# Performance work log

Hardware: AMD Instinct MI355X
Metric: run time of the kernel (lower is better)

The kernel has to match this reference:

```python
import jax, jax.numpy as jnp
import numpy as np

B, S, D = 16, 2048, 128


def setup_inputs() -> dict:
    key = jax.random.key(0)
    kq, kk, kv = jax.random.split(key, 3)
    return {
        "queries": jax.random.normal(kq, (B, S, D), dtype=jnp.float32),
        "keys": jax.random.normal(kk, (B, S, D), dtype=jnp.float32),
        "values": jax.random.normal(kv, (B, S, D), dtype=jnp.float32),
        "mask": jnp.zeros((B, S, S), dtype=bool),  # True -> masked out
    }


def reference(queries, keys, values, mask):
    d_k = queries.shape[-1]
    scale = 1.0 / np.sqrt(d_k).astype(np.float32)
    # scores: [B, S, S]
    scores = jnp.einsum("bqd,bkd->bqk", queries, keys) * scale
    scores = jnp.where(mask, -jnp.inf, scores)
    attn_weights = jax.nn.softmax(scores, axis=-1)
    # dropout prob = 0.0 (eval), identity
    output = jnp.einsum("bqk,bkd->bqd", attn_weights, values)
    return output
```

## Files before the change

kernel.cpp:

```cpp
#include <hip/hip_runtime.h>
#include <hip/hip_bf16.h>

#define SEQ    2048
#define DIM    128
#define NBATCH 16
#define KVB    64
#define HALFS  (SEQ / 2)
#define NTILE  (HALFS / KVB)
#define QW     32
#define NWAVE  4
#define QB     (QW * NWAVE)
#define NROW   (NBATCH * SEQ)
#define TELEM  (KVB * DIM)

typedef __bf16 bf16x8 __attribute__((ext_vector_type(8)));
typedef float  f32x4  __attribute__((ext_vector_type(4)));
typedef unsigned int uint;

#define LOG2E  1.44269504088896340736f
#define NEGINF (-__builtin_inff())

#define CVT_PK(d, lo, hi) asm("v_cvt_pk_bf16_f32 %0, %1, %2" : "=v"(d) : "v"(lo), "v"(hi))
#define SWAP32(x, y) asm("v_permlane32_swap_b32 %0, %1" : "+v"(x), "+v"(y))
#define SWAP16(x, y) asm("v_permlane16_swap_b32 %0, %1" : "+v"(x), "+v"(y))

typedef const __attribute__((address_space(1))) uint* gup;
typedef       __attribute__((address_space(3))) uint* lup;
#define GLDS16(g, l) __builtin_amdgcn_global_load_lds((gup)(g), (lup)(l), 16, 0, 0)

#define APPLY_MASK(mw, s)                          \
    if (mw) {                                      \
        if (mw & 0x000000ffu) s[0] = NEGINF;       \
        if (mw & 0x0000ff00u) s[1] = NEGINF;       \
        if (mw & 0x00ff0000u) s[2] = NEGINF;       \
        if (mw & 0xff000000u) s[3] = NEGINF;       \
    }

__global__ __launch_bounds__(512)
void sdpa_prep(const float* __restrict__ Kg, const float* __restrict__ Vg,
               __bf16* __restrict__ Kb, __bf16* __restrict__ Vb)
{
    const int tile = (int)blockIdx.x;
    const int tid  = (int)threadIdx.x;
    const size_t row0 = (size_t)tile * KVB;

    {
        const int kr = tid >> 3;
        const int c2 = (tid & 7) * 2;
        const int kx = kr & 7;
        const float* src = Kg + (row0 + kr) * DIM;
        __bf16* dst = Kb + ((size_t)tile * KVB + kr) * DIM;
        #pragma unroll
        for (int c = 0; c < 2; ++c) {
            const int ci = c2 + c;
            const int sc = ci ^ kx;
            const float4 a = *(const float4*)(src + sc * 8);
            const float4 b = *(const float4*)(src + sc * 8 + 4);
            bf16x8 h;
            h[0]=(__bf16)a.x; h[1]=(__bf16)a.y; h[2]=(__bf16)a.z; h[3]=(__bf16)a.w;
            h[4]=(__bf16)b.x; h[5]=(__bf16)b.y; h[6]=(__bf16)b.z; h[7]=(__bf16)b.w;
            *(bf16x8*)(dst + ci * 8) = h;
        }
    }
    {
        const int vd  = tid & 127;
        const int vks = tid >> 7;
        const int vx  = vd & 7;
        const float* src = Vg + row0 * DIM + vd;
        __bf16* dst = Vb + (size_t)tile * TELEM + (size_t)vd * KVB;
        #pragma unroll
        for (int c = 0; c < 2; ++c) {
            const int ck = vks * 2 + c;
            const int ci = ck ^ vx;
            bf16x8 h;
            #pragma unroll
            for (int j = 0; j < 8; ++j) h[j] = (__bf16)src[(size_t)(ck * 8 + j) * DIM];
            *(bf16x8*)(dst + ci * 8) = h;
        }
    }
}

__global__ __launch_bounds__(256, 2)
void sdpa_main(const float* __restrict__ Qg, const __bf16* __restrict__ Kbf,
               const __bf16* __restrict__ Vbf, const unsigned char* __restrict__ Mg,
               float* __restrict__ Uw, float* __restrict__ Lw)
{
    __shared__ __bf16 Ksh[2][TELEM];
    __shared__ __bf16 Vsh[2][TELEM];

    const int tid  = (int)threadIdx.x;
    const int wid  = tid >> 6;
    const int lane = tid & 63;
    const int lg   = lane >> 4;
    const int lr   = lane & 15;

    const int bid  = (int)blockIdx.x;
    const int nbid = (bid & 7) * 64 + (bid >> 3);
    const int half = nbid & 1;
    const int qt   = nbid >> 1;
    const int bb   = qt >> 4;
    const int q0w  = (qt & 15) * QB + wid * QW;

    const float qscale = 0.08838834764831845f * LOG2E;

    bf16x8 aqA[4], aqB[4];
    #pragma unroll
    for (int g = 0; g < 2; ++g) {
        const float* qrow = Qg + ((size_t)(bb * SEQ + q0w + g * 16 + lr)) * DIM;
        #pragma unroll
        for (int kb = 0; kb < 4; ++kb) {
            const float4 f0 = *(const float4*)(qrow + kb * 32 + lg * 8);
            const float4 f1 = *(const float4*)(qrow + kb * 32 + lg * 8 + 4);
            bf16x8 h;
            h[0] = (__bf16)(f0.x * qscale); h[1] = (__bf16)(f0.y * qscale);
            h[2] = (__bf16)(f0.z * qscale); h[3] = (__bf16)(f0.w * qscale);
            h[4] = (__bf16)(f1.x * qscale); h[5] = (__bf16)(f1.y * qscale);
            h[6] = (__bf16)(f1.z * qscale); h[7] = (__bf16)(f1.w * qscale);
            if (g == 0) aqA[kb] = h; else aqB[kb] = h;
        }
    }

    const __bf16* Kt0 = Kbf + (size_t)(bb * 32 + half * 16) * TELEM;
    const __bf16* Vt0 = Vbf + (size_t)(bb * 32 + half * 16) * TELEM;
    const unsigned char* MrowA = Mg + (size_t)bb * SEQ * SEQ
                               + (size_t)(q0w + lr) * SEQ + half * HALFS;
    const unsigned char* MrowB = MrowA + (size_t)16 * SEQ;

    uint mA0, mA1, mA2, mA3, mB0, mB1, mB2, mB3;
    const int loff = lane * 16;

    auto issue = [&](int t, int b) {
        const char* Ks = (const char*)(Kt0 + (size_t)t * TELEM);
        const char* Vs = (const char*)(Vt0 + (size_t)t * TELEM);
        char* Kd = (char*)Ksh[b];
        char* Vd = (char*)Vsh[b];
        #pragma unroll
        for (int j = 0; j < 4; ++j) {
            const int o = wid * 1024 + j * 4096;
            GLDS16(Ks + o + loff, Kd + o);
            GLDS16(Vs + o + loff, Vd + o);
        }
        const unsigned char* msA = MrowA + t * KVB + lg * 4;
        mA0 = *(const uint*)(msA);
        mA1 = *(const uint*)(msA + 16);
        mA2 = *(const uint*)(msA + 32);
        mA3 = *(const uint*)(msA + 48);
        const unsigned char* msB = MrowB + t * KVB + lg * 4;
        mB0 = *(const uint*)(msB);
        mB1 = *(const uint*)(msB + 16);
        mB2 = *(const uint*)(msB + 32);
        mB3 = *(const uint*)(msB + 48);
    };

    issue(0, 0);

    f32x4 accA[8], accB[8];
    #pragma unroll
    for (int i = 0; i < 8; ++i) { accA[i] = (f32x4)(0.0f); accB[i] = (f32x4)(0.0f); }
    float lA = 0.0f, lB = 0.0f;

    const int kxr = lr & 7;

    for (int t = 0; t < NTILE; ++t) {
        asm volatile("s_waitcnt vmcnt(0)" ::: "memory");
        __syncthreads();
        const uint wA0 = mA0, wA1 = mA1, wA2 = mA2, wA3 = mA3;
        const uint wB0 = mB0, wB1 = mB1, wB2 = mB2, wB3 = mB3;
        if (t + 1 < NTILE) issue(t + 1, (t + 1) & 1);

        const bf16x8* const Kc = (const bf16x8*)Ksh[t & 1];
        const bf16x8* const Vc = (const bf16x8*)Vsh[t & 1];

        f32x4 sA0 = (f32x4)(0.0f), sA1 = (f32x4)(0.0f);
        f32x4 sA2 = (f32x4)(0.0f), sA3 = (f32x4)(0.0f);
        f32x4 sB0 = (f32x4)(0.0f), sB1 = (f32x4)(0.0f);
        f32x4 sB2 = (f32x4)(0.0f), sB3 = (f32x4)(0.0f);
        __builtin_amdgcn_s_setprio(1);
        #pragma unroll
        for (int kb = 0; kb < 4; ++kb) {
            const int ch = (kb * 4 + lg) ^ kxr;
            const bf16x8 a0 = Kc[(lr)      * 16 + ch];
            const bf16x8 a1 = Kc[(16 + lr) * 16 + ch];
            const bf16x8 a2 = Kc[(32 + lr) * 16 + ch];
            const bf16x8 a3 = Kc[(48 + lr) * 16 + ch];
            sA0 = __builtin_amdgcn_mfma_f32_16x16x32_bf16(a0, aqA[kb], sA0, 0, 0, 0);
            sB0 = __builtin_amdgcn_mfma_f32_16x16x32_bf16(a0, aqB[kb], sB0, 0, 0, 0);
            sA1 = __builtin_amdgcn_mfma_f32_16x16x32_bf16(a1, aqA[kb], sA1, 0, 0, 0);
            sB1 = __builtin_amdgcn_mfma_f32_16x16x32_bf16(a1, aqB[kb], sB1, 0, 0, 0);
            sA2 = __builtin_amdgcn_mfma_f32_16x16x32_bf16(a2, aqA[kb], sA2, 0, 0, 0);
            sB2 = __builtin_amdgcn_mfma_f32_16x16x32_bf16(a2, aqB[kb], sB2, 0, 0, 0);
            sA3 = __builtin_amdgcn_mfma_f32_16x16x32_bf16(a3, aqA[kb], sA3, 0, 0, 0);
            sB3 = __builtin_amdgcn_mfma_f32_16x16x32_bf16(a3, aqB[kb], sB3, 0, 0, 0);
        }
        __builtin_amdgcn_s_setprio(0);

        APPLY_MASK(wA0, sA0) APPLY_MASK(wA1, sA1) APPLY_MASK(wA2, sA2) APPLY_MASK(wA3, sA3)
        APPLY_MASK(wB0, sB0) APPLY_MASK(wB1, sB1) APPLY_MASK(wB2, sB2) APPLY_MASK(wB3, sB3)

        float psA = 0.0f, psB = 0.0f;
        #pragma unroll
        for (int r = 0; r < 4; ++r) { sA0[r] = __builtin_amdgcn_exp2f(sA0[r]); psA += sA0[r]; }
        #pragma unroll
        for (int r = 0; r < 4; ++r) { sA1[r] = __builtin_amdgcn_exp2f(sA1[r]); psA += sA1[r]; }
        #pragma unroll
        for (int r = 0; r < 4; ++r) { sA2[r] = __builtin_amdgcn_exp2f(sA2[r]); psA += sA2[r]; }
        #pragma unroll
        for (int r = 0; r < 4; ++r) { sA3[r] = __builtin_amdgcn_exp2f(sA3[r]); psA += sA3[r]; }
        #pragma unroll
        for (int r = 0; r < 4; ++r) { sB0[r] = __builtin_amdgcn_exp2f(sB0[r]); psB += sB0[r]; }
        #pragma unroll
        for (int r = 0; r < 4; ++r) { sB1[r] = __builtin_amdgcn_exp2f(sB1[r]); psB += sB1[r]; }
        #pragma unroll
        for (int r = 0; r < 4; ++r) { sB2[r] = __builtin_amdgcn_exp2f(sB2[r]); psB += sB2[r]; }
        #pragma unroll
        for (int r = 0; r < 4; ++r) { sB3[r] = __builtin_amdgcn_exp2f(sB3[r]); psB += sB3[r]; }
        lA += psA;
        lB += psB;

        bf16x8 apA0, apA1, apB0, apB1;
        {
            uint a0w, a1w, b0w, b1w, c0w, c1w, d0w, d1w;
            CVT_PK(a0w, sA0[0], sA0[1]); CVT_PK(a1w, sA0[2], sA0[3]);
            CVT_PK(b0w, sA1[0], sA1[1]); CVT_PK(b1w, sA1[2], sA1[3]);
            CVT_PK(c0w, sA2[0], sA2[1]); CVT_PK(c1w, sA2[2], sA2[3]);
            CVT_PK(d0w, sA3[0], sA3[1]); CVT_PK(d1w, sA3[2], sA3[3]);
            SWAP32(a0w, b0w); SWAP16(a0w, b0w);
            SWAP32(a1w, b1w); SWAP16(a1w, b1w);
            SWAP32(c0w, d0w); SWAP16(c0w, d0w);
            SWAP32(c1w, d1w); SWAP16(c1w, d1w);
            union W { uint w[4]; bf16x8 v; };
            W u0, u1;
            u0.w[0] = a0w; u0.w[1] = a1w; u0.w[2] = b0w; u0.w[3] = b1w;
            u1.w[0] = c0w; u1.w[1] = c1w; u1.w[2] = d0w; u1.w[3] = d1w;
            apA0 = u0.v; apA1 = u1.v;
        }
        {
            uint a0w, a1w, b0w, b1w, c0w, c1w, d0w, d1w;
            CVT_PK(a0w, sB0[0], sB0[1]); CVT_PK(a1w, sB0[2], sB0[3]);
            CVT_PK(b0w, sB1[0], sB1[1]); CVT_PK(b1w, sB1[2], sB1[3]);
            CVT_PK(c0w, sB2[0], sB2[1]); CVT_PK(c1w, sB2[2], sB2[3]);
            CVT_PK(d0w, sB3[0], sB3[1]); CVT_PK(d1w, sB3[2], sB3[3]);
            SWAP32(a0w, b0w); SWAP16(a0w, b0w);
            SWAP32(a1w, b1w); SWAP16(a1w, b1w);
            SWAP32(c0w, d0w); SWAP16(c0w, d0w);
            SWAP32(c1w, d1w); SWAP16(c1w, d1w);
            union W { uint w[4]; bf16x8 v; };
            W u0, u1;
            u0.w[0] = a0w; u0.w[1] = a1w; u0.w[2] = b0w; u0.w[3] = b1w;
            u1.w[0] = c0w; u1.w[1] = c1w; u1.w[2] = d0w; u1.w[3] = d1w;
            apB0 = u0.v; apB1 = u1.v;
        }

        __builtin_amdgcn_s_setprio(1);
        #pragma unroll
        for (int nt = 0; nt < 8; ++nt) {
            const int rowb = (nt * 16 + lr) * 8;
            const bf16x8 bv0 = Vc[rowb + (lg ^ kxr)];
            const bf16x8 bv1 = Vc[rowb + ((4 + lg) ^ kxr)];
            accA[nt] = __builtin_amdgcn_mfma_f32_16x16x32_bf16(apA0, bv0, accA[nt], 0, 0, 0);
            accA[nt] = __builtin_amdgcn_mfma_f32_16x16x32_bf16(apA1, bv1, accA[nt], 0, 0, 0);
            accB[nt] = __builtin_amdgcn_mfma_f32_16x16x32_bf16(apB0, bv0, accB[nt], 0, 0, 0);
            accB[nt] = __builtin_amdgcn_mfma_f32_16x16x32_bf16(apB1, bv1, accB[nt], 0, 0, 0);
        }
        __builtin_amdgcn_s_setprio(0);
    }

    lA += __shfl_xor(lA, 16); lA += __shfl_xor(lA, 32);
    lB += __shfl_xor(lB, 16); lB += __shfl_xor(lB, 32);
    if (lg == 0) {
        Lw[(size_t)half * NROW + bb * SEQ + q0w + lr]      = lA;
        Lw[(size_t)half * NROW + bb * SEQ + q0w + 16 + lr] = lB;
    }

    float* ubA = Uw + ((size_t)half * NROW + bb * SEQ + q0w + lg * 4) * DIM + lr;
    float* ubB = ubA + (size_t)16 * DIM;
    #pragma unroll
    for (int r = 0; r < 4; ++r)
        #pragma unroll
        for (int nt = 0; nt < 8; ++nt) {
            ubA[(size_t)r * DIM + nt * 16] = accA[nt][r];
            ubB[(size_t)r * DIM + nt * 16] = accB[nt][r];
        }
}

__global__ __launch_bounds__(256)
void sdpa_combine(float* __restrict__ Og, const float* __restrict__ Uw,
                  const float* __restrict__ Lw)
{
    const int gid = (int)blockIdx.x * 256 + (int)threadIdx.x;
    const int row = gid >> 5;
    const float inv = 1.0f / (Lw[row] + Lw[NROW + row]);
    const float4* U0 = (const float4*)Uw;
    const float4* U1 = (const float4*)(Uw + (size_t)NROW * DIM);
    const float4 a = U0[gid];
    const float4 b = U1[gid];
    float4 o;
    o.x = (a.x + b.x) * inv; o.y = (a.y + b.y) * inv;
    o.z = (a.z + b.z) * inv; o.w = (a.w + b.w) * inv;
    ((float4*)Og)[gid] = o;
}

extern "C" void kernel_launch(void* const* d_in, const int* in_sizes, int n_in,
                              void* d_out, int out_size, void* d_ws, size_t ws_size,
                              hipStream_t stream) {
    const float* Q = (const float*)d_in[0];
    const float* K = (const float*)d_in[1];
    const float* V = (const float*)d_in[2];
    const unsigned char* M = (const unsigned char*)d_in[3];
    float* O  = (float*)d_out;
    float*  Uw  = (float*)d_ws;
    float*  Lw  = Uw + (size_t)2 * NROW * DIM;
    __bf16* Kbf = (__bf16*)(Lw + 2 * NROW);
    __bf16* Vbf = Kbf + (size_t)NROW * DIM;
    sdpa_prep<<<dim3(NROW / KVB), dim3(512), 0, stream>>>(K, V, Kbf, Vbf);
    sdpa_main<<<dim3(512), dim3(256), 0, stream>>>(Q, Kbf, Vbf, M, Uw, Lw);
    sdpa_combine<<<dim3(NROW * DIM / 4 / 256), dim3(256), 0, stream>>>(O, Uw, Lw);
}
```

Measured before the change: 76.44 us.

## Split KV sequence into four parts with 32-row tiles for more blocks

Splits the key/value range four ways instead of two, doubling the main-kernel grid to 1024 blocks, and shrinks KV tiles from 64 to 32 rows. This halves LDS use per block and raises the occupancy hint to 3 blocks per CU, aiming to fill the GPU better and hide latency. The cost is more partial-output traffic: four fp32 slabs are written and then read back in the combine kernel. Each tile also does less MFMA work per barrier, so per-tile sync overhead grows relative to compute. The V layout swizzle is changed to match the narrower tile.

After: 91.88 us. 20.2% more time.

```diff
diff --git a/kernel.cpp b/kernel.cpp
--- a/kernel.cpp
+++ b/kernel.cpp
@@ -4,9 +4,10 @@
 #define SEQ    2048
 #define DIM    128
 #define NBATCH 16
-#define KVB    64
-#define HALFS  (SEQ / 2)
-#define NTILE  (HALFS / KVB)
+#define KVB    32
+#define NSPLIT 4
+#define QUART  (SEQ / NSPLIT)
+#define NTILE  (QUART / KVB)
 #define QW     32
 #define NWAVE  4
 #define QB     (QW * NWAVE)
@@ -36,7 +37,7 @@
         if (mw & 0xff000000u) s[3] = NEGINF;       \
     }
 
-__global__ __launch_bounds__(512)
+__global__ __launch_bounds__(256)
 void sdpa_prep(const float* __restrict__ Kg, const float* __restrict__ Vg,
                __bf16* __restrict__ Kb, __bf16* __restrict__ Vb)
 {
@@ -49,7 +50,7 @@
         const int c2 = (tid & 7) * 2;
         const int kx = kr & 7;
         const float* src = Kg + (row0 + kr) * DIM;
-        __bf16* dst = Kb + ((size_t)tile * KVB + kr) * DIM;
+        __bf16* dst = Kb + (size_t)tile * TELEM + (size_t)kr * DIM;
         #pragma unroll
         for (int c = 0; c < 2; ++c) {
             const int ci = c2 + c;
@@ -63,14 +64,14 @@
         }
     }
     {
-        const int vd  = tid & 127;
-        const int vks = tid >> 7;
-        const int vx  = vd & 7;
+        const int vd = tid & 127;
+        const int cp = (tid >> 7) * 2;
+        const int vx = (vd >> 1) & 3;
         const float* src = Vg + row0 * DIM + vd;
         __bf16* dst = Vb + (size_t)tile * TELEM + (size_t)vd * KVB;
         #pragma unroll
         for (int c = 0; c < 2; ++c) {
-            const int ck = vks * 2 + c;
+            const int ck = cp + c;
             const int ci = ck ^ vx;
             bf16x8 h;
             #pragma unroll
@@ -80,7 +81,7 @@
     }
 }
 
-__global__ __launch_bounds__(256, 2)
+__global__ __launch_bounds__(256, 3)
 void sdpa_main(const float* __restrict__ Qg, const __bf16* __restrict__ Kbf,
                const __bf16* __restrict__ Vbf, const unsigned char* __restrict__ Mg,
                float* __restrict__ Uw, float* __restrict__ Lw)
@@ -95,18 +96,19 @@
     const int lr   = lane & 15;
 
     const int bid  = (int)blockIdx.x;
-    const int nbid = (bid & 7) * 64 + (bid >> 3);
-    const int half = nbid & 1;
-    const int qt   = nbid >> 1;
-    const int bb   = qt >> 4;
-    const int q0w  = (qt & 15) * QB + wid * QW;
+    const int nbid = (bid & 7) * 128 + (bid >> 3);
+    const int qtl  = nbid & 15;
+    const int g    = nbid >> 4;
+    const int quar = g & 3;
+    const int bb   = g >> 2;
+    const int q0w  = qtl * QB + wid * QW;
 
     const float qscale = 0.08838834764831845f * LOG2E;
 
     bf16x8 aqA[4], aqB[4];
     #pragma unroll
-    for (int g = 0; g < 2; ++g) {
-        const float* qrow = Qg + ((size_t)(bb * SEQ + q0w + g * 16 + lr)) * DIM;
+    for (int gq = 0; gq < 2; ++gq) {
+        const float* qrow = Qg + ((size_t)(bb * SEQ + q0w + gq * 16 + lr)) * DIM;
         #pragma unroll
         for (int kb = 0; kb < 4; ++kb) {
             const float4 f0 = *(const float4*)(qrow + kb * 32 + lg * 8);
@@ -116,17 +118,17 @@
             h[2] = (__bf16)(f0.z * qscale); h[3] = (__bf16)(f0.w * qscale);
             h[4] = (__bf16)(f1.x * qscale); h[5] = (__bf16)(f1.y * qscale);
             h[6] = (__bf16)(f1.z * qscale); h[7] = (__bf16)(f1.w * qscale);
-            if (g == 0) aqA[kb] = h; else aqB[kb] = h;
-        }
-    }
-
-    const __bf16* Kt0 = Kbf + (size_t)(bb * 32 + half * 16) * TELEM;
-    const __bf16* Vt0 = Vbf + (size_t)(bb * 32 + half * 16) * TELEM;
+            if (gq == 0) aqA[kb] = h; else aqB[kb] = h;
+        }
+    }
+
+    const __bf16* Kt0 = Kbf + (size_t)(bb * 64 + quar * 16) * TELEM;
+    const __bf16* Vt0 = Vbf + (size_t)(bb * 64 + quar * 16) * TELEM;
     const unsigned char* MrowA = Mg + (size_t)bb * SEQ * SEQ
-                               + (size_t)(q0w + lr) * SEQ + half * HALFS;
+                               + (size_t)(q0w + lr) * SEQ + quar * QUART;
     const unsigned char* MrowB = MrowA + (size_t)16 * SEQ;
 
-    uint mA0, mA1, mA2, mA3, mB0, mB1, mB2, mB3;
+    uint mA0, mA1, mB0, mB1;
     const int loff = lane * 16;
 
     auto issue = [&](int t, int b) {
@@ -135,7 +137,7 @@
         char* Kd = (char*)Ksh[b];
         char* Vd = (char*)Vsh[b];
         #pragma unroll
-        for (int j = 0; j < 4; ++j) {
+        for (int j = 0; j < 2; ++j) {
             const int o = wid * 1024 + j * 4096;
             GLDS16(Ks + o + loff, Kd + o);
             GLDS16(Vs + o + loff, Vd + o);
@@ -143,13 +145,9 @@
         const unsigned char* msA = MrowA + t * KVB + lg * 4;
         mA0 = *(const uint*)(msA);
         mA1 = *(const uint*)(msA + 16);
-        mA2 = *(const uint*)(msA + 32);
-        mA3 = *(const uint*)(msA + 48);
         const unsigned char* msB = MrowB + t * KVB + lg * 4;
         mB0 = *(const uint*)(msB);
         mB1 = *(const uint*)(msB + 16);
-        mB2 = *(const uint*)(msB + 32);
-        mB3 = *(const uint*)(msB + 48);
     };
 
     issue(0, 0);
@@ -160,42 +158,34 @@
     float lA = 0.0f, lB = 0.0f;
 
     const int kxr = lr & 7;
+    const int vxr = (lr >> 1) & 3;
 
     for (int t = 0; t < NTILE; ++t) {
         asm volatile("s_waitcnt vmcnt(0)" ::: "memory");
         __syncthreads();
-        const uint wA0 = mA0, wA1 = mA1, wA2 = mA2, wA3 = mA3;
-        const uint wB0 = mB0, wB1 = mB1, wB2 = mB2, wB3 = mB3;
+        const uint wA0 = mA0, wA1 = mA1, wB0 = mB0, wB1 = mB1;
         if (t + 1 < NTILE) issue(t + 1, (t + 1) & 1);
 
         const bf16x8* const Kc = (const bf16x8*)Ksh[t & 1];
         const bf16x8* const Vc = (const bf16x8*)Vsh[t & 1];
 
         f32x4 sA0 = (f32x4)(0.0f), sA1 = (f32x4)(0.0f);
-        f32x4 sA2 = (f32x4)(0.0f), sA3 = (f32x4)(0.0f);
         f32x4 sB0 = (f32x4)(0.0f), sB1 = (f32x4)(0.0f);
-        f32x4 sB2 = (f32x4)(0.0f), sB3 = (f32x4)(0.0f);
         __builtin_amdgcn_s_setprio(1);
         #pragma unroll
         for (int kb = 0; kb < 4; ++kb) {
             const int ch = (kb * 4 + lg) ^ kxr;
             const bf16x8 a0 = Kc[(lr)      * 16 + ch];
             const bf16x8 a1 = Kc[(16 + lr) * 16 + ch];
-            const bf16x8 a2 = Kc[(32 + lr) * 16 + ch];
-            const bf16x8 a3 = Kc[(48 + lr) * 16 + ch];
             sA0 = __builtin_amdgcn_mfma_f32_16x16x32_bf16(a0, aqA[kb], sA0, 0, 0, 0);
             sB0 = __builtin_amdgcn_mfma_f32_16x16x32_bf16(a0, aqB[kb], sB0, 0, 0, 0);
             sA1 = __builtin_amdgcn_mfma_f32_16x16x32_bf16(a1, aqA[kb], sA1, 0, 0, 0);
             sB1 = __builtin_amdgcn_mfma_f32_16x16x32_bf16(a1, aqB[kb], sB1, 0, 0, 0);
-            sA2 = __builtin_amdgcn_mfma_f32_16x16x32_bf16(a2, aqA[kb], sA2, 0, 0, 0);
-            sB2 = __builtin_amdgcn_mfma_f32_16x16x32_bf16(a2, aqB[kb], sB2, 0, 0, 0);
-            sA3 = __builtin_amdgcn_mfma_f32_16x16x32_bf16(a3, aqA[kb], sA3, 0, 0, 0);
-            sB3 = __builtin_amdgcn_mfma_f32_16x16x32_bf16(a3, aqB[kb], sB3, 0, 0, 0);
         }
         __builtin_amdgcn_s_setprio(0);
 
-        APPLY_MASK(wA0, sA0) APPLY_MASK(wA1, sA1) APPLY_MASK(wA2, sA2) APPLY_MASK(wA3, sA3)
-        APPLY_MASK(wB0, sB0) APPLY_MASK(wB1, sB1) APPLY_MASK(wB2, sB2) APPLY_MASK(wB3, sB3)
+        APPLY_MASK(wA0, sA0) APPLY_MASK(wA1, sA1)
+        APPLY_MASK(wB0, sB0) APPLY_MASK(wB1, sB1)
 
         float psA = 0.0f, psB = 0.0f;
         #pragma unroll
@@ -203,64 +193,40 @@
         #pragma unroll
         for (int r = 0; r < 4; ++r) { sA1[r] = __builtin_amdgcn_exp2f(sA1[r]); psA += sA1[r]; }
         #pragma unroll
-        for (int r = 0; r < 4; ++r) { sA2[r] = __builtin_amdgcn_exp2f(sA2[r]); psA += sA2[r]; }
-        #pragma unroll
-        for (int r = 0; r < 4; ++r) { sA3[r] = __builtin_amdgcn_exp2f(sA3[r]); psA += sA3[r]; }
-        #pragma unroll
         for (int r = 0; r < 4; ++r) { sB0[r] = __builtin_amdgcn_exp2f(sB0[r]); psB += sB0[r]; }
         #pragma unroll
         for (int r = 0; r < 4; ++r) { sB1[r] = __builtin_amdgcn_exp2f(sB1[r]); psB += sB1[r]; }
-        #pragma unroll
-        for (int r = 0; r < 4; ++r) { sB2[r] = __builtin_amdgcn_exp2f(sB2[r]); psB += sB2[r]; }
-        #pragma unroll
-        for (int r = 0; r < 4; ++r) { sB3[r] = __builtin_amdgcn_exp2f(sB3[r]); psB += sB3[r]; }
         lA += psA;
         lB += psB;
 
-        bf16x8 apA0, apA1, apB0, apB1;
+        bf16x8 apA, apB;
         {
-            uint a0w, a1w, b0w, b1w, c0w, c1w, d0w, d1w;
+            uint a0w, a1w, b0w, b1w;
             CVT_PK(a0w, sA0[0], sA0[1]); CVT_PK(a1w, sA0[2], sA0[3]);
             CVT_PK(b0w, sA1[0], sA1[1]); CVT_PK(b1w, sA1[2], sA1[3]);
-            CVT_PK(c0w, sA2[0], sA2[1]); CVT_PK(c1w, sA2[2], sA2[3]);
-            CVT_PK(d0w, sA3[0], sA3[1]); CVT_PK(d1w, sA3[2], sA3[3]);
             SWAP32(a0w, b0w); SWAP16(a0w, b0w);
             SWAP32(a1w, b1w); SWAP16(a1w, b1w);
-            SWAP32(c0w, d0w); SWAP16(c0w, d0w);
-            SWAP32(c1w, d1w); SWAP16(c1w, d1w);
-            union W { uint w[4]; bf16x8 v; };
-            W u0, u1;
-            u0.w[0] = a0w; u0.w[1] = a1w; u0.w[2] = b0w; u0.w[3] = b1w;
-            u1.w[0] = c0w; u1.w[1] = c1w; u1.w[2] = d0w; u1.w[3] = d1w;
-            apA0 = u0.v; apA1 = u1.v;
+            union W { uint w[4]; bf16x8 v; } u;
+            u.w[0] = a0w; u.w[1] = a1w; u.w[2] = b0w; u.w[3] = b1w;
+            apA = u.v;
         }
         {
-            uint a0w, a1w, b0w, b1w, c0w, c1w, d0w, d1w;
+            uint a0w, a1w, b0w, b1w;
             CVT_PK(a0w, sB0[0], sB0[1]); CVT_PK(a1w, sB0[2], sB0[3]);
             CVT_PK(b0w, sB1[0], sB1[1]); CVT_PK(b1w, sB1[2], sB1[3]);
-            CVT_PK(c0w, sB2[0], sB2[1]); CVT_PK(c1w, sB2[2], sB2[3]);
-            CVT_PK(d0w, sB3[0], sB3[1]); CVT_PK(d1w, sB3[2], sB3[3]);
             SWAP32(a0w, b0w); SWAP16(a0w, b0w);
             SWAP32(a1w, b1w); SWAP16(a1w, b1w);
-            SWAP32(c0w, d0w); SWAP16(c0w, d0w);
-            SWAP32(c1w, d1w); SWAP16(c1w, d1w);
-            union W { uint w[4]; bf16x8 v; };
-            W u0, u1;
-            u0.w[0] = a0w; u0.w[1] = a1w; u0.w[2] = b0w; u0.w[3] = b1w;
-            u1.w[0] = c0w; u1.w[1] = c1w; u1.w[2] = d0w; u1.w[3] = d1w;
-            apB0 = u0.v; apB1 = u1.v;
+            union W { uint w[4]; bf16x8 v; } u;
+            u.w[0] = a0w; u.w[1] = a1w; u.w[2] = b0w; u.w[3] = b1w;
+            apB = u.v;
         }
 
         __builtin_amdgcn_s_setprio(1);
         #pragma unroll
         for (int nt = 0; nt < 8; ++nt) {
-            const int rowb = (nt * 16 + lr) * 8;
-            const bf16x8 bv0 = Vc[rowb + (lg ^ kxr)];
-            const bf16x8 bv1 = Vc[rowb + ((4 + lg) ^ kxr)];
-            accA[nt] = __builtin_amdgcn_mfma_f32_16x16x32_bf16(apA0, bv0, accA[nt], 0, 0, 0);
-            accA[nt] = __builtin_amdgcn_mfma_f32_16x16x32_bf16(apA1, bv1, accA[nt], 0, 0, 0);
-            accB[nt] = __builtin_amdgcn_mfma_f32_16x16x32_bf16(apB0, bv0, accB[nt], 0, 0, 0);
-            accB[nt] = __builtin_amdgcn_mfma_f32_16x16x32_bf16(apB1, bv1, accB[nt], 0, 0, 0);
+            const bf16x8 bv = Vc[(nt * 16 + lr) * 4 + (lg ^ vxr)];
+            accA[nt] = __builtin_amdgcn_mfma_f32_16x16x32_bf16(apA, bv, accA[nt], 0, 0, 0);
+            accB[nt] = __builtin_amdgcn_mfma_f32_16x16x32_bf16(apB, bv, accB[nt], 0, 0, 0);
         }
         __builtin_amdgcn_s_setprio(0);
     }
@@ -268,11 +234,11 @@
     lA += __shfl_xor(lA, 16); lA += __shfl_xor(lA, 32);
     lB += __shfl_xor(lB, 16); lB += __shfl_xor(lB, 32);
     if (lg == 0) {
-        Lw[(size_t)half * NROW + bb * SEQ + q0w + lr]      = lA;
-        Lw[(size_t)half * NROW + bb * SEQ + q0w + 16 + lr] = lB;
-    }
-
-    float* ubA = Uw + ((size_t)half * NROW + bb * SEQ + q0w + lg * 4) * DIM + lr;
+        Lw[(size_t)quar * NROW + bb * SEQ + q0w + lr]      = lA;
+        Lw[(size_t)quar * NROW + bb * SEQ + q0w + 16 + lr] = lB;
+    }
+
+    float* ubA = Uw + ((size_t)quar * NROW + bb * SEQ + q0w + lg * 4) * DIM + lr;
     float* ubB = ubA + (size_t)16 * DIM;
     #pragma unroll
     for (int r = 0; r < 4; ++r)
@@ -289,14 +255,19 @@
 {
     const int gid = (int)blockIdx.x * 256 + (int)threadIdx.x;
     const int row = gid >> 5;
-    const float inv = 1.0f / (Lw[row] + Lw[NROW + row]);
-    const float4* U0 = (const float4*)Uw;
-    const float4* U1 = (const float4*)(Uw + (size_t)NROW * DIM);
-    const float4 a = U0[gid];
-    const float4 b = U1[gid];
+    const float inv = 1.0f / (Lw[row] + Lw[NROW + row]
+                            + Lw[2 * NROW + row] + Lw[3 * (size_t)NROW + row]);
+    const size_t slab = (size_t)NROW * DIM / 4;
+    const float4* U = (const float4*)Uw;
+    const float4 a = U[gid];
+    const float4 b = U[slab + gid];
+    const float4 c = U[2 * slab + gid];
+    const float4 d = U[3 * slab + gid];
     float4 o;
-    o.x = (a.x + b.x) * inv; o.y = (a.y + b.y) * inv;
-    o.z = (a.z + b.z) * inv; o.w = (a.w + b.w) * inv;
+    o.x = (a.x + b.x + c.x + d.x) * inv;
+    o.y = (a.y + b.y + c.y + d.y) * inv;
+    o.z = (a.z + b.z + c.z + d.z) * inv;
+    o.w = (a.w + b.w + c.w + d.w) * inv;
     ((float4*)Og)[gid] = o;
 }
 
@@ -309,10 +280,10 @@
     const unsigned char* M = (const unsigned char*)d_in[3];
     float* O  = (float*)d_out;
     float*  Uw  = (float*)d_ws;
-    float*  Lw  = Uw + (size_t)2 * NROW * DIM;
-    __bf16* Kbf = (__bf16*)(Lw + 2 * NROW);
+    float*  Lw  = Uw + (size_t)NSPLIT * NROW * DIM;
+    __bf16* Kbf = (__bf16*)(Lw + (size_t)NSPLIT * NROW);
     __bf16* Vbf = Kbf + (size_t)NROW * DIM;
-    sdpa_prep<<<dim3(NROW / KVB), dim3(512), 0, stream>>>(K, V, Kbf, Vbf);
-    sdpa_main<<<dim3(512), dim3(256), 0, stream>>>(Q, Kbf, Vbf, M, Uw, Lw);
+    sdpa_prep<<<dim3(NROW / KVB), dim3(256), 0, stream>>>(K, V, Kbf, Vbf);
+    sdpa_main<<<dim3(NBATCH * 16 * NSPLIT), dim3(256), 0, stream>>>(Q, Kbf, Vbf, M, Uw, Lw);
     sdpa_combine<<<dim3(NROW * DIM / 4 / 256), dim3(256), 0, stream>>>(O, Uw, Lw);
 }
```
